# Optimization experiments

Measured on AMD Instinct MI355X. Metric: run time of the kernel, lower is better.

The kernel has to match this reference:

```python
import jax, jax.numpy as jnp
import numpy as np

DEGREE = 30
ORDER = 3                      # cubic-ish B-spline order used by the module
N_COEF = DEGREE + ORDER - 1    # 32 coefficients, matches compute_starting_values
SPLINE_RANGE = (-15.0, 15.0)
SPAN_FACTOR = 0.1
LOG_2PI = float(np.log(2.0 * np.pi))


def _knots():
    """Uniform knot grid expanded by span_factor, as in gtm's bspline helpers."""
    rmin, rmax = SPLINE_RANGE
    pad = (rmax - rmin) * SPAN_FACTOR
    lo, hi = rmin - pad, rmax + pad
    dist = (hi - lo) / (N_COEF - ORDER)
    i = jnp.arange(N_COEF + ORDER + 1, dtype=jnp.float32)
    return lo + (i - ORDER) * dist, lo, dist


def _deboor(x, span, knots, coefs, p):
    """Vectorized deBoor: x [N], span [N] with knots[span] <= x < knots[span+1]."""
    d = [coefs[span - p + j] for j in range(p + 1)]  # gather p+1 local coefs
    for r in range(1, p + 1):
        for j in range(p, r - 1, -1):
            kl = knots[span + j - p]
            kr = knots[span + 1 + j - r]
            alpha = (x - kl) / (kr - kl)
            d[j] = (1.0 - alpha) * d[j - 1] + alpha * d[j]
    return d[p]


def _bspline_value_and_deriv(params, y):
    # monotonic restriction: c0 = params[0], c_k = c0 + sum softplus(params[1:k+1])
    coefs = jnp.concatenate(
        [params[:1], params[0] + jnp.cumsum(jax.nn.softplus(params[1:]))]
    )
    knots, lo, dist = _knots()
    # 'reluler' span restriction: clamp inputs into the spline range
    x = jnp.clip(y, SPLINE_RANGE[0], SPLINE_RANGE[1])
    span = jnp.clip(
        jnp.floor((x - lo) / dist).astype(jnp.int32) + ORDER, ORDER, N_COEF - 1
    )
    val = _deboor(x, span, knots, coefs, ORDER)
    # derivative spline: degree p-1, coefs p*(c[i+1]-c[i])/(t[i+p+1]-t[i+1])
    dcoefs = ORDER * (coefs[1:] - coefs[:-1]) / (
        knots[ORDER + 1 : ORDER + N_COEF] - knots[1:N_COEF]
    )
    der = _deboor(x, span - 1, knots[1:-1], dcoefs, ORDER - 1)
    return val, der


def setup_inputs() -> dict:
    key = jax.random.key(0)
    k1, k2 = jax.random.split(key)
    params = jax.random.normal(k1, (N_COEF,), dtype=jnp.float32)
    y = jax.random.normal(k2, (20_000_000,), dtype=jnp.float32)
    return {"params": params, "y": y}


def reference(params, y):
    z_tilde, der_1 = _bspline_value_and_deriv(params, y)
    # Normal(0,1).log_prob(z) + log(der_1)
    return -0.5 * z_tilde * z_tilde - 0.5 * LOG_2PI + jnp.log(der_1)
```

## Files before the change

### kernel.cpp

```cpp
#include <hip/hip_runtime.h>
#include <math.h>

#define SP_INV_DIST (29.0f / 36.0f)
#define SP_U_OFFS   (17.5f)
#define NEG_HALF_LOG_2PI (-0.91893853320467274f)

__global__ void TM_precompute(const float* __restrict__ params,
                              float* __restrict__ ws) {
    __shared__ float sp[32];
    __shared__ float c[32];
    int t = threadIdx.x;
    if (t >= 1 && t < 32) {
        float p = params[t];
        sp[t] = (p > 0.0f) ? (p + log1pf(expf(-p))) : log1pf(expf(p));
    }
    __syncthreads();
    if (t == 0) {
        float acc = params[0];
        c[0] = acc;
        for (int k = 1; k < 32; ++k) { acc += sp[k]; c[k] = acc; }
    }
    __syncthreads();
    if (t < 32) {
        float4 vp = make_float4(0.f, 0.f, 0.f, 0.f);
        float4 dp = make_float4(0.f, 0.f, 0.f, 0.f);
        if (t >= 3) {
            float d0 = c[t - 3], d1 = c[t - 2], d2 = c[t - 1], d3 = c[t];
            const float SIXTH = 1.0f / 6.0f;
            float a0 = (d0 + 4.0f * d1 + d2) * SIXTH;
            float a1 = (d2 - d0) * 0.5f;
            float a2 = (d0 - 2.0f * d1 + d2) * 0.5f;
            float a3 = (d3 - d0 + 3.0f * (d1 - d2)) * SIXTH;
            vp = make_float4(a0, a1, a2, a3);
            dp = make_float4(a1 * SP_INV_DIST,
                             2.0f * a2 * SP_INV_DIST,
                             3.0f * a3 * SP_INV_DIST, 0.0f);
        }
        float4* ws4 = reinterpret_cast<float4*>(ws);
        ws4[t]      = vp;
        ws4[32 + t] = dp;
    }
}

__device__ __forceinline__ float eval_one(float xin, const float4* __restrict__ tab) {
    float x = fminf(fmaxf(xin, -15.0f), 15.0f);
    float u = fmaf(x, SP_INV_DIST, SP_U_OFFS);
    int   s = (int)u;
    s = min(max(s, 3), 31);
    float f = u - (float)s;
    float4 a = tab[s];
    float4 q = tab[32 + s];
    float val = fmaf(fmaf(fmaf(a.w, f, a.z), f, a.y), f, a.x);
    float der = fmaf(fmaf(q.z, f, q.y), f, q.x);
    return fmaf(-0.5f * val, val, NEG_HALF_LOG_2PI) + __logf(der);
}

__global__ __launch_bounds__(256) void TM_73727408603569_kernel(
        const float* __restrict__ y, const float* __restrict__ ws,
        float* __restrict__ out, int n4, int tail_base, int tail) {
    __shared__ float s_tab[256];
    int t = threadIdx.x;
    s_tab[t] = ws[t];
    __syncthreads();
    const float4* tab = reinterpret_cast<const float4*>(s_tab);

    const float4* y4 = reinterpret_cast<const float4*>(y);
    float4*       o4 = reinterpret_cast<float4*>(out);

    int i0 = blockIdx.x * 512 + t;
    int i1 = i0 + 256;
    bool p0 = i0 < n4, p1 = i1 < n4;
    float4 v0, v1;
    if (p0) v0 = y4[i0];
    if (p1) v1 = y4[i1];
    if (p0) {
        float4 r;
        r.x = eval_one(v0.x, tab); r.y = eval_one(v0.y, tab);
        r.z = eval_one(v0.z, tab); r.w = eval_one(v0.w, tab);
        o4[i0] = r;
    }
    if (p1) {
        float4 r;
        r.x = eval_one(v1.x, tab); r.y = eval_one(v1.y, tab);
        r.z = eval_one(v1.z, tab); r.w = eval_one(v1.w, tab);
        o4[i1] = r;
    }

    if (blockIdx.x == 0 && t < tail) {
        int idx = tail_base + t;
        out[idx] = eval_one(y[idx], tab);
    }
}

extern "C" void kernel_launch(void* const* d_in, const int* in_sizes, int n_in,
                              void* d_out, int out_size, void* d_ws, size_t ws_size,
                              hipStream_t stream) {
    const float* params = (const float*)d_in[0];
    const float* y      = (const float*)d_in[1];
    float*       out    = (float*)d_out;
    float*       ws     = (float*)d_ws;
    int n  = in_sizes[1];
    int n4 = n >> 2;
    int tail = n & 3;

    TM_precompute<<<1, 64, 0, stream>>>(params, ws);

    int blocks = (n4 + 511) / 512;
    if (blocks < 1) blocks = 1;
    TM_73727408603569_kernel<<<blocks, 256, 0, stream>>>(y, ws, out, n4,
                                                         n4 << 2, tail);
}
```

Before: 34.50 us.

## Fuse coefficient precompute into main kernel, derive derivative inline, use nontemporal IO

Drops the separate single-block precompute launch. Each block now builds the cubic coefficient table itself, using a wavefront shuffle prefix sum over the softplus terms. The derivative polynomial is computed inline from the value coefficients, so only one table lookup is needed per element, and the span clamp is removed. Each thread now handles four float4 vectors with nontemporal loads and stores, cutting launch overhead and table traffic at the cost of redundant per-block setup and fewer blocks.

```diff
diff --git a/kernel.cpp b/kernel.cpp
--- a/kernel.cpp
+++ b/kernel.cpp
@@ -5,85 +5,90 @@
 #define SP_U_OFFS   (17.5f)
 #define NEG_HALF_LOG_2PI (-0.91893853320467274f)
 
-__global__ void TM_precompute(const float* __restrict__ params,
-                              float* __restrict__ ws) {
-    __shared__ float sp[32];
-    __shared__ float c[32];
-    int t = threadIdx.x;
-    if (t >= 1 && t < 32) {
-        float p = params[t];
-        sp[t] = (p > 0.0f) ? (p + log1pf(expf(-p))) : log1pf(expf(p));
-    }
-    __syncthreads();
-    if (t == 0) {
-        float acc = params[0];
-        c[0] = acc;
-        for (int k = 1; k < 32; ++k) { acc += sp[k]; c[k] = acc; }
-    }
-    __syncthreads();
-    if (t < 32) {
-        float4 vp = make_float4(0.f, 0.f, 0.f, 0.f);
-        float4 dp = make_float4(0.f, 0.f, 0.f, 0.f);
-        if (t >= 3) {
-            float d0 = c[t - 3], d1 = c[t - 2], d2 = c[t - 1], d3 = c[t];
-            const float SIXTH = 1.0f / 6.0f;
-            float a0 = (d0 + 4.0f * d1 + d2) * SIXTH;
-            float a1 = (d2 - d0) * 0.5f;
-            float a2 = (d0 - 2.0f * d1 + d2) * 0.5f;
-            float a3 = (d3 - d0 + 3.0f * (d1 - d2)) * SIXTH;
-            vp = make_float4(a0, a1, a2, a3);
-            dp = make_float4(a1 * SP_INV_DIST,
-                             2.0f * a2 * SP_INV_DIST,
-                             3.0f * a3 * SP_INV_DIST, 0.0f);
-        }
-        float4* ws4 = reinterpret_cast<float4*>(ws);
-        ws4[t]      = vp;
-        ws4[32 + t] = dp;
-    }
-}
+typedef float f32x4 __attribute__((ext_vector_type(4)));
 
 __device__ __forceinline__ float eval_one(float xin, const float4* __restrict__ tab) {
     float x = fminf(fmaxf(xin, -15.0f), 15.0f);
     float u = fmaf(x, SP_INV_DIST, SP_U_OFFS);
     int   s = (int)u;
-    s = min(max(s, 3), 31);
     float f = u - (float)s;
     float4 a = tab[s];
-    float4 q = tab[32 + s];
     float val = fmaf(fmaf(fmaf(a.w, f, a.z), f, a.y), f, a.x);
-    float der = fmaf(fmaf(q.z, f, q.y), f, q.x);
+    float der = fmaf(f, fmaf(f, 3.0f * a.w, 2.0f * a.z), a.y) * SP_INV_DIST;
     return fmaf(-0.5f * val, val, NEG_HALF_LOG_2PI) + __logf(der);
 }
 
 __global__ __launch_bounds__(256) void TM_73727408603569_kernel(
-        const float* __restrict__ y, const float* __restrict__ ws,
+        const float* __restrict__ y, const float* __restrict__ params,
         float* __restrict__ out, int n4, int tail_base, int tail) {
-    __shared__ float s_tab[256];
+    __shared__ float4 tab[32];
     int t = threadIdx.x;
-    s_tab[t] = ws[t];
+
+    if (t < 64) {
+        bool lane_p = (t >= 1 && t < 32);
+        float p  = lane_p ? params[t] : 0.0f;
+        float sp = lane_p ? ((p > 0.0f) ? (p + log1pf(expf(-p)))
+                                        : log1pf(expf(p)))
+                          : 0.0f;
+        #pragma unroll
+        for (int d = 1; d < 32; d <<= 1) {
+            float o = __shfl_up(sp, d, 64);
+            if (t >= d) sp += o;
+        }
+        float c  = params[0] + sp;
+        float d0 = __shfl_up(c, 3, 64);
+        float d1 = __shfl_up(c, 2, 64);
+        float d2 = __shfl_up(c, 1, 64);
+        float d3 = c;
+        if (t < 32) {
+            float4 vp = make_float4(0.f, 0.f, 0.f, 0.f);
+            if (t >= 3) {
+                const float SIXTH = 1.0f / 6.0f;
+                vp.x = (d0 + 4.0f * d1 + d2) * SIXTH;
+                vp.y = (d2 - d0) * 0.5f;
+                vp.z = (d0 - 2.0f * d1 + d2) * 0.5f;
+                vp.w = (d3 - d0 + 3.0f * (d1 - d2)) * SIXTH;
+            }
+            tab[t] = vp;
+        }
+    }
     __syncthreads();
-    const float4* tab = reinterpret_cast<const float4*>(s_tab);
 
-    const float4* y4 = reinterpret_cast<const float4*>(y);
-    float4*       o4 = reinterpret_cast<float4*>(out);
+    const f32x4* y4 = reinterpret_cast<const f32x4*>(y);
+    f32x4*       o4 = reinterpret_cast<f32x4*>(out);
 
-    int i0 = blockIdx.x * 512 + t;
-    int i1 = i0 + 256;
-    bool p0 = i0 < n4, p1 = i1 < n4;
-    float4 v0, v1;
-    if (p0) v0 = y4[i0];
-    if (p1) v1 = y4[i1];
+    int i0 = blockIdx.x * 1024 + t;
+    int i1 = i0 + 256, i2 = i0 + 512, i3 = i0 + 768;
+    bool p0 = i0 < n4, p1 = i1 < n4, p2 = i2 < n4, p3 = i3 < n4;
+    f32x4 v0, v1, v2, v3;
+    if (p0) v0 = __builtin_nontemporal_load(&y4[i0]);
+    if (p1) v1 = __builtin_nontemporal_load(&y4[i1]);
+    if (p2) v2 = __builtin_nontemporal_load(&y4[i2]);
+    if (p3) v3 = __builtin_nontemporal_load(&y4[i3]);
+
     if (p0) {
-        float4 r;
+        f32x4 r;
         r.x = eval_one(v0.x, tab); r.y = eval_one(v0.y, tab);
         r.z = eval_one(v0.z, tab); r.w = eval_one(v0.w, tab);
-        o4[i0] = r;
+        __builtin_nontemporal_store(r, &o4[i0]);
     }
     if (p1) {
-        float4 r;
+        f32x4 r;
         r.x = eval_one(v1.x, tab); r.y = eval_one(v1.y, tab);
         r.z = eval_one(v1.z, tab); r.w = eval_one(v1.w, tab);
-        o4[i1] = r;
+        __builtin_nontemporal_store(r, &o4[i1]);
+    }
+    if (p2) {
+        f32x4 r;
+        r.x = eval_one(v2.x, tab); r.y = eval_one(v2.y, tab);
+        r.z = eval_one(v2.z, tab); r.w = eval_one(v2.w, tab);
+        __builtin_nontemporal_store(r, &o4[i2]);
+    }
+    if (p3) {
+        f32x4 r;
+        r.x = eval_one(v3.x, tab); r.y = eval_one(v3.y, tab);
+        r.z = eval_one(v3.z, tab); r.w = eval_one(v3.w, tab);
+        __builtin_nontemporal_store(r, &o4[i3]);
     }
 
     if (blockIdx.x == 0 && t < tail) {
@@ -98,15 +103,12 @@
     const float* params = (const float*)d_in[0];
     const float* y      = (const float*)d_in[1];
     float*       out    = (float*)d_out;
-    float*       ws     = (float*)d_ws;
-    int n  = in_sizes[1];
-    int n4 = n >> 2;
+    int n    = in_sizes[1];
+    int n4   = n >> 2;
     int tail = n & 3;
 
-    TM_precompute<<<1, 64, 0, stream>>>(params, ws);
-
-    int blocks = (n4 + 511) / 512;
+    int blocks = (n4 + 1023) / 1024;
     if (blocks < 1) blocks = 1;
-    TM_73727408603569_kernel<<<blocks, 256, 0, stream>>>(y, ws, out, n4,
+    TM_73727408603569_kernel<<<blocks, 256, 0, stream>>>(y, params, out, n4,
                                                          n4 << 2, tail);
 }
```

Measured after the change: 35.90 us. 4.1% more time.
